# Performance work log

Measured on AMD Instinct MI355X. Metric: run time of the kernel, lower is better.

## Reference

```python
import jax, jax.numpy as jnp
import numpy as np

MI_N, DIS_N = 16384, 8192
EM = 128
E_MM, E_DD = MI_N * 32, DIS_N * 32


def _add_self_loops(edges, ew, n):
    loop = jnp.arange(n, dtype=edges.dtype)
    row = jnp.concatenate([edges[0], loop])
    col = jnp.concatenate([edges[1], loop])
    ew = jnp.concatenate([ew, jnp.ones((n,), ew.dtype)])
    return row, col, ew


def gcn_conv(x, edges, w, b, n, ew=None):
    # PyG GCNConv: symmetric gcn_norm with self-loops (fill 1.0), then
    # out[col] += norm * (x @ w)[row], plus bias.
    if ew is None:
        ew = jnp.ones((edges.shape[1],), x.dtype)
    row, col, ew = _add_self_loops(edges, ew, n)
    deg = jax.ops.segment_sum(ew, col, num_segments=n)
    dinv = jnp.where(deg > 0, jax.lax.rsqrt(deg), 0.0)
    norm = dinv[row] * ew * dinv[col]          # [E+n]
    h = x @ w                                   # [n, d]
    return jax.ops.segment_sum(h[row] * norm[:, None], col, num_segments=n) + b


def gat_conv(x, edges, w, a_src, a_dst, b, n):
    # PyG GATConv, heads=1: per-edge attention LeakyReLU(0.2) + softmax over
    # incoming edges of each target node (self-loops added).
    h = x @ w                                   # [n, d]
    row, col, _ = _add_self_loops(edges, jnp.ones((edges.shape[1],), x.dtype), n)
    e = jax.nn.leaky_relu((h @ a_src)[row] + (h @ a_dst)[col], negative_slope=0.2)
    m = jax.ops.segment_max(e, col, num_segments=n)
    ex = jnp.exp(e - m[col])
    s = jax.ops.segment_sum(ex, col, num_segments=n)
    alpha = ex / s[col]                         # [E+n]
    return jax.ops.segment_sum(h[row] * alpha[:, None], col, num_segments=n) + b


def setup_inputs() -> dict:
    key = jax.random.key(0)
    ks = jax.random.split(key, 24)
    sc = 1.0 / np.sqrt(EM)
    d = {
        'mm_x0': jax.random.normal(ks[0], (MI_N, EM), jnp.float32),
        'dd_x0': jax.random.normal(ks[1], (DIS_N, EM), jnp.float32),
        'w1_mm': jax.random.normal(ks[2], (EM, EM), jnp.float32) * sc,
        'b1_mm': jnp.zeros((EM,), jnp.float32),
        'w2_mm': jax.random.normal(ks[3], (EM, EM), jnp.float32) * sc,
        'b2_mm': jnp.zeros((EM,), jnp.float32),
        'w3_mm': jax.random.normal(ks[4], (EM, EM), jnp.float32) * sc,
        'asrc_mm': jax.random.normal(ks[5], (EM,), jnp.float32) * sc,
        'adst_mm': jax.random.normal(ks[6], (EM,), jnp.float32) * sc,
        'b3_mm': jnp.zeros((EM,), jnp.float32),
        'w1_dd': jax.random.normal(ks[7], (EM, EM), jnp.float32) * sc,
        'b1_dd': jnp.zeros((EM,), jnp.float32),
        'w2_dd': jax.random.normal(ks[8], (EM, EM), jnp.float32) * sc,
        'b2_dd': jnp.zeros((EM,), jnp.float32),
        'w3_dd': jax.random.normal(ks[9], (EM, EM), jnp.float32) * sc,
        'asrc_dd': jax.random.normal(ks[10], (EM,), jnp.float32) * sc,
        'adst_dd': jax.random.normal(ks[11], (EM,), jnp.float32) * sc,
        'b3_dd': jnp.zeros((EM,), jnp.float32),
        'mm_ew': jax.random.uniform(ks[12], (E_MM,), jnp.float32),
        'dd_ew': jax.random.uniform(ks[13], (E_DD,), jnp.float32),
        'mm_edges': jax.random.randint(ks[14], (2, E_MM), 0, MI_N, jnp.int32),
        'dd_edges': jax.random.randint(ks[15], (2, E_DD), 0, DIS_N, jnp.int32),
    }
    return d


def reference(mm_x0, dd_x0, w1_mm, b1_mm, w2_mm, b2_mm, w3_mm, asrc_mm, adst_mm,
              b3_mm, w1_dd, b1_dd, w2_dd, b2_dd, w3_dd, asrc_dd, adst_dd, b3_dd,
              mm_ew, dd_ew, mm_edges, dd_edges):
    elu = jax.nn.elu
    m1 = elu(gcn_conv(mm_x0, mm_edges, w1_mm, b1_mm, MI_N, mm_ew))
    m2 = elu(gcn_conv(m1, mm_edges, w2_mm, b2_mm, MI_N))
    m3 = elu(gat_conv(m2, mm_edges, w3_mm, asrc_mm, adst_mm, b3_mm, MI_N))
    d1 = elu(gcn_conv(dd_x0, dd_edges, w1_dd, b1_dd, DIS_N, dd_ew))
    d2 = elu(gcn_conv(d1, dd_edges, w2_dd, b2_dd, DIS_N))
    d3 = elu(gat_conv(d2, dd_edges, w3_dd, asrc_dd, adst_dd, b3_dd, DIS_N))
    mi_fea = (m1 + m2 + m3) / 3.0
    dis_fea = (d1 + d2 + d3) / 3.0
    score_raw = mi_fea @ dis_fea.T              # [MI_N, DIS_N]
    mn, mx = jnp.min(score_raw), jnp.max(score_raw)
    denom = jnp.where(mx > mn, mx - mn, jnp.asarray(1.0, score_raw.dtype))
    score_norm = jnp.where(mx > mn, (score_raw - mn) / denom,
                           jnp.zeros_like(score_raw))
    score_norm = jnp.clip(score_norm, 0.0, 1.0)
    return score_norm, mi_fea, dis_fea
```

## Files before the change

### kernel.cpp

```cpp
#include <hip/hip_runtime.h>
#include <cstdint>
#include <cstddef>

#define MI_NN 16384
#define DIS_NN 8192
#define EMB 128
#define EMM (MI_NN*32)
#define EDD (DIS_NN*32)

typedef __attribute__((ext_vector_type(8))) short short8;
typedef __attribute__((ext_vector_type(4))) float f32x4;

__device__ __forceinline__ float leakyr(float x){ return x > 0.f ? x : 0.2f*x; }
__device__ __forceinline__ float eluf(float x){ return x > 0.f ? x : expm1f(x); }

__device__ __forceinline__ unsigned bf16u(float x){
  unsigned u = __float_as_uint(x);
  return (u + 0x7FFFu + ((u >> 16) & 1u)) >> 16;
}
__device__ __forceinline__ float bfl(unsigned p){ return __uint_as_float(p << 16); }
__device__ __forceinline__ float bfh(unsigned p){ return __uint_as_float(p & 0xFFFF0000u); }

__global__ __launch_bounds__(256) void k_count2g(const int* __restrict__ c0, int* __restrict__ n0c,
                                                 int E0, int nb0,
                                                 const int* __restrict__ c1, int* __restrict__ n1c,
                                                 int E1){
  int b = blockIdx.x;
  const int* col; int* cnt; int E; int t;
  if (b < nb0){ col = c0; cnt = n0c; E = E0; t = b*256 + threadIdx.x; }
  else        { col = c1; cnt = n1c; E = E1; t = (b - nb0)*256 + threadIdx.x; }
  if (t < E) atomicAdd(&cnt[col[t]], 1);
}

__global__ __launch_bounds__(1024) void k_scan2g(const int* __restrict__ cnt0, int* __restrict__ rp0,
                                                 int n0, int E0,
                                                 const int* __restrict__ cnt1, int* __restrict__ rp1,
                                                 int n1, int E1){
  const int* cnt = blockIdx.x ? cnt1 : cnt0;
  int* rowptr    = blockIdx.x ? rp1  : rp0;
  int n          = blockIdx.x ? n1   : n0;
  int E          = blockIdx.x ? E1   : E0;
  __shared__ int lds[1024];
  int t = threadIdx.x;
  int chunk = n >> 10;
  int base = t*chunk;
  int s = 0;
  for (int i = 0; i < chunk; ++i) s += cnt[base+i];
  lds[t] = s; __syncthreads();
  for (int off = 1; off < 1024; off <<= 1){
    int v = (t >= off) ? lds[t-off] : 0;
    __syncthreads();
    lds[t] += v;
    __syncthreads();
  }
  int run = lds[t] - s;
  for (int i = 0; i < chunk; ++i){ rowptr[base+i] = run; run += cnt[base+i]; }
  if (t == 0) rowptr[n] = E;
}

__global__ __launch_bounds__(256) void k_fill2g(
    const int* __restrict__ r0a, const int* __restrict__ c0a, const float* __restrict__ w0a,
    const int* __restrict__ rp0, int* __restrict__ f0, int* __restrict__ s0, float* __restrict__ v0,
    int E0, int nb0,
    const int* __restrict__ r1a, const int* __restrict__ c1a, const float* __restrict__ w1a,
    const int* __restrict__ rp1, int* __restrict__ f1, int* __restrict__ s1, float* __restrict__ v1,
    int E1){
  int b = blockIdx.x;
  const int *row, *col; const float* ew; const int* rowptr;
  int *fill, *esrc; float* ewv; int E, t;
  if (b < nb0){ row=r0a; col=c0a; ew=w0a; rowptr=rp0; fill=f0; esrc=s0; ewv=v0; E=E0; t=b*256+threadIdx.x; }
  else        { row=r1a; col=c1a; ew=w1a; rowptr=rp1; fill=f1; esrc=s1; ewv=v1; E=E1; t=(b-nb0)*256+threadIdx.x; }
  if (t < E){
    int c = col[t];
    int p = rowptr[c] + atomicAdd(&fill[c], 1);
    esrc[p] = row[t];
    ewv[p] = ew[t];
  }
}

__global__ __launch_bounds__(256) void k_gemm2g(const float* __restrict__ X0, const float* __restrict__ W0,
                                                ushort* __restrict__ H0, int nb0,
                                                const float* __restrict__ X1, const float* __restrict__ W1,
                                                ushort* __restrict__ H1){
  int b = blockIdx.x;
  const float *X, *W; ushort* H; int rb;
  if (b < nb0){ X = X0; W = W0; H = H0; rb = b; }
  else        { X = X1; W = W1; H = H1; rb = b - nb0; }
  __shared__ float wl[EMB*EMB];
  int t = threadIdx.x;
  {
    const float4* W4 = (const float4*)W;
    float4* L4 = (float4*)wl;
    #pragma unroll
    for (int i = 0; i < 16; ++i) L4[t + 256*i] = W4[t + 256*i];
  }
  __syncthreads();
  int jg = t & 31;
  int rg = t >> 5;
  int r0 = rb*32 + rg*4;
  f32x4 acc0 = {0,0,0,0}, acc1 = {0,0,0,0}, acc2 = {0,0,0,0}, acc3 = {0,0,0,0};
  const float4* X4 = (const float4*)X;
  for (int k4 = 0; k4 < 32; ++k4){
    float4 x0 = X4[(size_t)(r0+0)*32 + k4];
    float4 x1 = X4[(size_t)(r0+1)*32 + k4];
    float4 x2 = X4[(size_t)(r0+2)*32 + k4];
    float4 x3 = X4[(size_t)(r0+3)*32 + k4];
#define GSTEP(c0,c1,c2,c3,kq) { f32x4 w4 = *(const f32x4*)&wl[(kq)*EMB + jg*4]; \
      acc0 += (c0)*w4; acc1 += (c1)*w4; acc2 += (c2)*w4; acc3 += (c3)*w4; }
    GSTEP(x0.x, x1.x, x2.x, x3.x, k4*4+0)
    GSTEP(x0.y, x1.y, x2.y, x3.y, k4*4+1)
    GSTEP(x0.z, x1.z, x2.z, x3.z, k4*4+2)
    GSTEP(x0.w, x1.w, x2.w, x3.w, k4*4+3)
#undef GSTEP
  }
#define PACK2(o, a) { o.x = bf16u(a[0]) | (bf16u(a[1])<<16); o.y = bf16u(a[2]) | (bf16u(a[3])<<16); }
  uint2 o0, o1, o2, o3;
  PACK2(o0, acc0) PACK2(o1, acc1) PACK2(o2, acc2) PACK2(o3, acc3)
#undef PACK2
  ushort* out = H + (size_t)r0*EMB + jg*4;
  *(uint2*)(out)         = o0;
  *(uint2*)(out + EMB)   = o1;
  *(uint2*)(out + 2*EMB) = o2;
  *(uint2*)(out + 3*EMB) = o3;
}

__global__ __launch_bounds__(256) void k_deg1_2g(const int* __restrict__ rp0, const float* __restrict__ ew0,
                                                 float* __restrict__ d0, int n0, int nb0,
                                                 const int* __restrict__ rp1, const float* __restrict__ ew1,
                                                 float* __restrict__ d1, int n1){
  int b = blockIdx.x;
  const int* rowptr; const float* ewv; float* dinv; int n, wid;
  int lane = threadIdx.x & 63;
  if (b < nb0){ rowptr=rp0; ewv=ew0; dinv=d0; n=n0; wid = (b*256 + threadIdx.x) >> 6; }
  else        { rowptr=rp1; ewv=ew1; dinv=d1; n=n1; wid = ((b-nb0)*256 + threadIdx.x) >> 6; }
  if (wid >= n) return;
  int beg = rowptr[wid], end = rowptr[wid+1];
  float s = 0.f;
  for (int i = beg + lane; i < end; i += 64) s += ewv[i];
  #pragma unroll
  for (int off = 32; off; off >>= 1) s += __shfl_xor(s, off);
  if (lane == 0) dinv[wid] = rsqrtf(1.0f + s);
}

__global__ __launch_bounds__(256) void k_deg2_2g(const int* __restrict__ rp0, float* __restrict__ d0,
                                                 int n0, int nb0,
                                                 const int* __restrict__ rp1, float* __restrict__ d1,
                                                 int n1){
  int b = blockIdx.x;
  const int* rowptr; float* dinv; int n, v;
  if (b < nb0){ rowptr=rp0; dinv=d0; n=n0; v = b*256 + threadIdx.x; }
  else        { rowptr=rp1; dinv=d1; n=n1; v = (b-nb0)*256 + threadIdx.x; }
  if (v < n) dinv[v] = rsqrtf(1.0f + (float)(rowptr[v+1] - rowptr[v]));
}

__global__ __launch_bounds__(256) void k_agg2g(
    const ushort* __restrict__ H0, const float* __restrict__ di0, const int* __restrict__ rp0,
    const int* __restrict__ sr0, const float* __restrict__ ew0, const float* __restrict__ bi0,
    float* __restrict__ xn0, float* __restrict__ fe0, int n0, int nb0,
    const ushort* __restrict__ H1, const float* __restrict__ di1, const int* __restrict__ rp1,
    const int* __restrict__ sr1, const float* __restrict__ ew1, const float* __restrict__ bi1,
    float* __restrict__ xn1, float* __restrict__ fe1, int n1,
    int femode){
  int b = blockIdx.x;
  const ushort* H; const float* dinv; const int* rowptr; const int* esrc;
  const float* ewv; const float* bias; float* xnext; float* fea; int n, wid;
  int lane = threadIdx.x & 63;
  if (b < nb0){ H=H0; dinv=di0; rowptr=rp0; esrc=sr0; ewv=ew0; bias=bi0; xnext=xn0; fea=fe0; n=n0;
                wid = (b*256 + threadIdx.x) >> 6; }
  else        { H=H1; dinv=di1; rowptr=rp1; esrc=sr1; ewv=ew1; bias=bi1; xnext=xn1; fea=fe1; n=n1;
                wid = ((b-nb0)*256 + threadIdx.x) >> 6; }
  if (wid >= n) return;
  int v = wid;
  float dv = dinv[v];
  unsigned hb = *(const unsigned*)(H + (size_t)v*EMB + lane*2);
  float ax = dv*bfl(hb), ay = dv*bfh(hb);
  int beg = rowptr[v], end = rowptr[v+1];
  int i = beg;
  int e4 = beg + ((end - beg) & ~3);
  for (; i < e4; i += 4){
    int r0 = esrc[i], r1 = esrc[i+1], r2 = esrc[i+2], r3 = esrc[i+3];
    float n0v = dinv[r0], n1v = dinv[r1], n2v = dinv[r2], n3v = dinv[r3];
    if (ewv){ n0v *= ewv[i]; n1v *= ewv[i+1]; n2v *= ewv[i+2]; n3v *= ewv[i+3]; }
    unsigned h0 = *(const unsigned*)(H + (size_t)r0*EMB + lane*2);
    unsigned h1 = *(const unsigned*)(H + (size_t)r1*EMB + lane*2);
    unsigned h2 = *(const unsigned*)(H + (size_t)r2*EMB + lane*2);
    unsigned h3 = *(const unsigned*)(H + (size_t)r3*EMB + lane*2);
    ax += n0v*bfl(h0) + n1v*bfl(h1) + n2v*bfl(h2) + n3v*bfl(h3);
    ay += n0v*bfh(h0) + n1v*bfh(h1) + n2v*bfh(h2) + n3v*bfh(h3);
  }
  for (; i < end; ++i){
    int r = esrc[i];
    float nm = dinv[r];
    if (ewv) nm *= ewv[i];
    unsigned hr = *(const unsigned*)(H + (size_t)r*EMB + lane*2);
    ax += nm*bfl(hr); ay += nm*bfh(hr);
  }
  float2 b2 = ((const float2*)bias)[lane];
  float ox = eluf(dv*ax + b2.x), oy = eluf(dv*ay + b2.y);
  ((float2*)xnext)[(size_t)v*64 + lane] = make_float2(ox, oy);
  float2* F2 = (float2*)fea;
  if (femode == 0){
    F2[(size_t)v*64 + lane] = make_float2(ox, oy);
  } else {
    float2 f = F2[(size_t)v*64 + lane];
    F2[(size_t)v*64 + lane] = make_float2(f.x + ox, f.y + oy);
  }
}

__global__ __launch_bounds__(256) void k_srcdst2g(
    const ushort* __restrict__ H0, const float* __restrict__ as0, const float* __restrict__ ad0,
    float* __restrict__ es0, float* __restrict__ ed0, int n0, int nb0,
    const ushort* __restrict__ H1, const float* __restrict__ as1, const float* __restrict__ ad1,
    float* __restrict__ es1, float* __restrict__ ed1, int n1){
  int b = blockIdx.x;
  const ushort* H; const float *asr, *ads; float *es, *ed; int n, wid;
  int lane = threadIdx.x & 63;
  if (b < nb0){ H=H0; asr=as0; ads=ad0; es=es0; ed=ed0; n=n0; wid = (b*256 + threadIdx.x) >> 6; }
  else        { H=H1; asr=as1; ads=ad1; es=es1; ed=ed1; n=n1; wid = ((b-nb0)*256 + threadIdx.x) >> 6; }
  if (wid >= n) return;
  unsigned hb = *(const unsigned*)(H + (size_t)wid*EMB + lane*2);
  float hx = bfl(hb), hy = bfh(hb);
  float2 s2 = ((const float2*)asr)[lane];
  float2 d2 = ((const float2*)ads)[lane];
  float ps = hx*s2.x + hy*s2.y;
  float pd = hx*d2.x + hy*d2.y;
  #pragma unroll
  for (int off = 32; off; off >>= 1){
    ps += __shfl_xor(ps, off);
    pd += __shfl_xor(pd, off);
  }
  if (lane == 0){ es[wid] = ps; ed[wid] = pd; }
}

__global__ __launch_bounds__(256) void k_gat2g(
    const ushort* __restrict__ H0, const float* __restrict__ es0, const float* __restrict__ ed0,
    const int* __restrict__ rp0, const int* __restrict__ sr0, const float* __restrict__ bi0,
    float* __restrict__ fe0, unsigned* __restrict__ sh0, int n0, int nb0,
    const ushort* __restrict__ H1, const float* __restrict__ es1, const float* __restrict__ ed1,
    const int* __restrict__ rp1, const int* __restrict__ sr1, const float* __restrict__ bi1,
    float* __restrict__ fe1, unsigned* __restrict__ sh1, int n1){
  int b = blockIdx.x;
  const ushort* H; const float *es, *ed; const int *rowptr, *esrc; const float* bias;
  float* fea; unsigned* shadow; int n, wid;
  int lane = threadIdx.x & 63;
  if (b < nb0){ H=H0; es=es0; ed=ed0; rowptr=rp0; esrc=sr0; bias=bi0; fea=fe0; shadow=sh0; n=n0;
                wid = (b*256 + threadIdx.x) >> 6; }
  else        { H=H1; es=es1; ed=ed1; rowptr=rp1; esrc=sr1; bias=bi1; fea=fe1; shadow=sh1; n=n1;
                wid = ((b-nb0)*256 + threadIdx.x) >> 6; }
  if (wid >= n) return;
  int v = wid;
  float edv = ed[v];
  float self_e = leakyr(es[v] + edv);
  int beg = rowptr[v], end = rowptr[v+1];
  float m = -3.4e38f, s = 0.f;
  for (int i = beg + lane; i < end; i += 64){
    float e = leakyr(es[esrc[i]] + edv);
    if (e > m){ s = s*expf(m - e) + 1.0f; m = e; }
    else s += expf(e - m);
  }
  #pragma unroll
  for (int off = 32; off; off >>= 1){
    float m2 = __shfl_xor(m, off), s2 = __shfl_xor(s, off);
    float mn_ = fmaxf(m, m2);
    s = s*expf(m - mn_) + s2*expf(m2 - mn_);
    m = mn_;
  }
  {
    float mn_ = fmaxf(m, self_e);
    s = s*expf(m - mn_) + expf(self_e - mn_);
    m = mn_;
  }
  float inv_s = 1.0f / s;
  unsigned hb = *(const unsigned*)(H + (size_t)v*EMB + lane*2);
  float a0 = expf(self_e - m)*inv_s;
  float ax = a0*bfl(hb), ay = a0*bfh(hb);
  int i = beg;
  int e4 = beg + ((end - beg) & ~3);
  for (; i < e4; i += 4){
    int r0 = esrc[i], r1 = esrc[i+1], r2 = esrc[i+2], r3 = esrc[i+3];
    float a_0 = expf(leakyr(es[r0] + edv) - m)*inv_s;
    float a_1 = expf(leakyr(es[r1] + edv) - m)*inv_s;
    float a_2 = expf(leakyr(es[r2] + edv) - m)*inv_s;
    float a_3 = expf(leakyr(es[r3] + edv) - m)*inv_s;
    unsigned h0 = *(const unsigned*)(H + (size_t)r0*EMB + lane*2);
    unsigned h1 = *(const unsigned*)(H + (size_t)r1*EMB + lane*2);
    unsigned h2 = *(const unsigned*)(H + (size_t)r2*EMB + lane*2);
    unsigned h3 = *(const unsigned*)(H + (size_t)r3*EMB + lane*2);
    ax += a_0*bfl(h0) + a_1*bfl(h1) + a_2*bfl(h2) + a_3*bfl(h3);
    ay += a_0*bfh(h0) + a_1*bfh(h1) + a_2*bfh(h2) + a_3*bfh(h3);
  }
  for (; i < end; ++i){
    int r = esrc[i];
    float a = expf(leakyr(es[r] + edv) - m)*inv_s;
    unsigned hr = *(const unsigned*)(H + (size_t)r*EMB + lane*2);
    ax += a*bfl(hr); ay += a*bfh(hr);
  }
  float2 b2 = ((const float2*)bias)[lane];
  float ox = eluf(ax + b2.x), oy = eluf(ay + b2.y);
  float2* F2 = (float2*)fea;
  float2 f = F2[(size_t)v*64 + lane];
  float fx = (f.x + ox)/3.0f, fy = (f.y + oy)/3.0f;
  F2[(size_t)v*64 + lane] = make_float2(fx, fy);
  shadow[(size_t)v*64 + lane] = bf16u(fx) | (bf16u(fy) << 16);
}

__device__ __forceinline__ void stage128(const uint8_t* G, uint8_t* L, int w, int lane){
  #pragma unroll
  for (int c = 0; c < 8; ++c){
    int linear = w*8192 + c*1024 + lane*16;
    int row = linear >> 8, col = linear & 255;
    const void* src = G + row*256 + (col ^ ((row & 7) << 4));
    __builtin_amdgcn_global_load_lds(
        (const __attribute__((address_space(1))) void*)src,
        (__attribute__((address_space(3))) void*)(L + w*8192 + c*1024),
        16, 0, 0);
  }
}

#define NT 16
template<int STORE>
__global__ __launch_bounds__(256) void k_score5(const ushort* __restrict__ Abf,
                                                const ushort* __restrict__ Bbf,
                                                float* __restrict__ S,
                                                float* __restrict__ mmpart){
  __shared__ __align__(16) uint8_t L0[32768];
  __shared__ __align__(16) uint8_t L1[32768];
  __shared__ float red[16];
  const int t = threadIdx.x;
  const int lane = t & 63;
  const int w = t >> 6;
  const int wr = w >> 1, wc = w & 1;
  const int lr = lane & 15, lk = lane >> 4;
  const int i0b = blockIdx.y * 128;
  const int jbase = blockIdx.x * NT;

  stage128((const uint8_t*)(Abf + (size_t)i0b*EMB), L0, w, lane);
  stage128((const uint8_t*)(Bbf + (size_t)jbase*128*EMB), L1, w, lane);
  __syncthreads();

  short8 af[4][4];
  #pragma unroll
  for (int at = 0; at < 4; ++at){
    int ra = wr*64 + at*16 + lr;
    #pragma unroll
    for (int k0 = 0; k0 < 4; ++k0){
      int kb = k0*64 + lk*16;
      af[at][k0] = *(const short8*)&L0[ra*256 + (kb ^ ((ra & 7) << 4))];
    }
  }
  __syncthreads();
  stage128((const uint8_t*)(Bbf + (size_t)(jbase+1)*128*EMB), L0, w, lane);

  float mn = 0.f, sc = 0.f;
  if (STORE){
    mn = mmpart[0];
    float mx = mmpart[1];
    sc = (mx > mn) ? 1.0f/(mx - mn) : 0.0f;
  }
  float lmin = 3.4e38f, lmax = -3.4e38f;

  for (int jt = 0; jt < NT; ++jt){
    uint8_t* curB = (jt & 1) ? L0 : L1;
    f32x4 acc[4][4];
    #pragma unroll
    for (int a = 0; a < 4; ++a)
      #pragma unroll
      for (int b = 0; b < 4; ++b) acc[a][b] = (f32x4){0.f,0.f,0.f,0.f};

    #pragma unroll
    for (int k0 = 0; k0 < 4; ++k0){
      int kb = k0*64 + lk*16;
      short8 bfr[4];
      #pragma unroll
      for (int ct = 0; ct < 4; ++ct){
        int rb = wc*64 + ct*16 + lr;
        bfr[ct] = *(const short8*)&curB[rb*256 + (kb ^ ((rb & 7) << 4))];
      }
      #pragma unroll
      for (int at = 0; at < 4; ++at)
        #pragma unroll
        for (int ct = 0; ct < 4; ++ct)
          acc[at][ct] = __builtin_amdgcn_mfma_f32_16x16x32_bf16(af[at][k0], bfr[ct], acc[at][ct], 0, 0, 0);
    }

    int j0 = (jbase + jt)*128;
    if (STORE){
      #pragma unroll
      for (int at = 0; at < 4; ++at){
        #pragma unroll
        for (int ct = 0; ct < 4; ++ct){
          int colj = j0 + wc*64 + ct*16 + lr;
          int row0 = i0b + wr*64 + at*16 + lk*4;
          #pragma unroll
          for (int q = 0; q < 4; ++q){
            float vv = fminf(fmaxf((acc[at][ct][q] - mn)*sc, 0.f), 1.f);
            S[(size_t)(row0+q)*DIS_NN + colj] = vv;
          }
        }
      }
    } else {
      #pragma unroll
      for (int at = 0; at < 4; ++at)
        #pragma unroll
        for (int ct = 0; ct < 4; ++ct)
          #pragma unroll
          for (int q = 0; q < 4; ++q){
            float vv = acc[at][ct][q];
            lmin = fminf(lmin, vv); lmax = fmaxf(lmax, vv);
          }
    }
    __syncthreads();
    if (jt + 2 < NT)
      stage128((const uint8_t*)(Bbf + (size_t)(jbase+jt+2)*128*EMB), curB, w, lane);
  }

  if (!STORE){
    #pragma unroll
    for (int off = 32; off; off >>= 1){
      lmin = fminf(lmin, __shfl_xor(lmin, off));
      lmax = fmaxf(lmax, __shfl_xor(lmax, off));
    }
    if (lane == 0){ red[w*2] = lmin; red[w*2+1] = lmax; }
    __syncthreads();
    if (t == 0){
      float a = fminf(fminf(red[0], red[2]), fminf(red[4], red[6]));
      float b = fmaxf(fmaxf(red[1], red[3]), fmaxf(red[5], red[7]));
      int bid = blockIdx.y * 4 + blockIdx.x;
      mmpart[2 + bid*2]     = a;
      mmpart[2 + bid*2 + 1] = b;
    }
  }
}

__global__ __launch_bounds__(512) void k_mmred(float* __restrict__ mm){
  __shared__ float2 red[8];
  int t = threadIdx.x;
  float mn = mm[2 + t*2];
  float mx = mm[2 + t*2 + 1];
  #pragma unroll
  for (int off = 32; off; off >>= 1){
    mn = fminf(mn, __shfl_xor(mn, off));
    mx = fmaxf(mx, __shfl_xor(mx, off));
  }
  if ((t & 63) == 0) red[t >> 6] = make_float2(mn, mx);
  __syncthreads();
  if (t == 0){
    float a = red[0].x, b = red[0].y;
    #pragma unroll
    for (int i = 1; i < 8; ++i){ a = fminf(a, red[i].x); b = fmaxf(b, red[i].y); }
    mm[0] = a; mm[1] = b;
  }
}

extern "C" void kernel_launch(void* const* d_in, const int* in_sizes, int n_in,
                              void* d_out, int out_size, void* d_ws, size_t ws_size,
                              hipStream_t stream){
  (void)in_sizes; (void)n_in; (void)out_size; (void)ws_size;
  const float* mm_x0  = (const float*)d_in[0];
  const float* dd_x0  = (const float*)d_in[1];
  const float* w1_mm  = (const float*)d_in[2];
  const float* b1_mm  = (const float*)d_in[3];
  const float* w2_mm  = (const float*)d_in[4];
  const float* b2_mm  = (const float*)d_in[5];
  const float* w3_mm  = (const float*)d_in[6];
  const float* asrc_mm= (const float*)d_in[7];
  const float* adst_mm= (const float*)d_in[8];
  const float* b3_mm  = (const float*)d_in[9];
  const float* w1_dd  = (const float*)d_in[10];
  const float* b1_dd  = (const float*)d_in[11];
  const float* w2_dd  = (const float*)d_in[12];
  const float* b2_dd  = (const float*)d_in[13];
  const float* w3_dd  = (const float*)d_in[14];
  const float* asrc_dd= (const float*)d_in[15];
  const float* adst_dd= (const float*)d_in[16];
  const float* b3_dd  = (const float*)d_in[17];
  const float* mm_ew  = (const float*)d_in[18];
  const float* dd_ew  = (const float*)d_in[19];
  const int* mm_edges = (const int*)d_in[20];
  const int* dd_edges = (const int*)d_in[21];

  float* S = (float*)d_out;
  float* p = S;
  float* A0m = p;  p += (size_t)MI_NN*EMB;
  float* A1m = p;  p += (size_t)MI_NN*EMB;
  float* A0d = p;  p += (size_t)DIS_NN*EMB;
  float* A1d = p;  p += (size_t)DIS_NN*EMB;
  ushort* Hbm = (ushort*)p; p += (size_t)MI_NN*EMB/2;
  ushort* Hbd = (ushort*)p; p += (size_t)DIS_NN*EMB/2;
  float* DEG1m = p; p += MI_NN;
  float* DEG2m = p; p += MI_NN;
  float* ESm   = p; p += MI_NN;
  float* EDm   = p; p += MI_NN;
  float* DEG1d = p; p += DIS_NN;
  float* DEG2d = p; p += DIS_NN;
  float* ESd   = p; p += DIS_NN;
  float* EDd   = p; p += DIS_NN;
  int* CNTm  = (int*)p; p += MI_NN;
  int* CNTd  = (int*)p; p += DIS_NN;
  int* FILLm = (int*)p; p += MI_NN;
  int* FILLd = (int*)p; p += DIS_NN;
  int* RPm   = (int*)p; p += MI_NN + 64;
  int* RPd   = (int*)p; p += DIS_NN + 64;
  int* ESRCm = (int*)p; p += EMM;
  int* ESRCd = (int*)p; p += EDD;
  float* EWVm = p; p += EMM;
  float* EWVd = p; p += EDD;
  float* FEA_MI  = S + (size_t)MI_NN * DIS_NN;
  float* FEA_DIS = FEA_MI + (size_t)MI_NN*EMB;

  float* MM = (float*)d_ws;
  ushort* Abf = (ushort*)((char*)d_ws + 16384);
  ushort* Bbf = Abf + (size_t)MI_NN * EMB;

  const int* erow_m = mm_edges;
  const int* ecol_m = mm_edges + EMM;
  const int* erow_d = dd_edges;
  const int* ecol_d = dd_edges + EDD;

  hipMemsetAsync(CNTm, 0, (size_t)(MI_NN + DIS_NN)*sizeof(int), stream);
  k_count2g<<<EMM/256 + EDD/256, 256, 0, stream>>>(ecol_m, CNTm, EMM, EMM/256,
                                                   ecol_d, CNTd, EDD);
  k_scan2g<<<2, 1024, 0, stream>>>(CNTm, RPm, MI_NN, EMM, CNTd, RPd, DIS_NN, EDD);
  hipMemsetAsync(FILLm, 0, (size_t)(MI_NN + DIS_NN)*sizeof(int), stream);
  k_fill2g<<<EMM/256 + EDD/256, 256, 0, stream>>>(erow_m, ecol_m, mm_ew, RPm, FILLm, ESRCm, EWVm,
                                                  EMM, EMM/256,
                                                  erow_d, ecol_d, dd_ew, RPd, FILLd, ESRCd, EWVd,
                                                  EDD);
  const int GB = MI_NN/32 + DIS_NN/32;
  const int AB = MI_NN/4 + DIS_NN/4;
  k_gemm2g<<<GB, 256, 0, stream>>>(mm_x0, w1_mm, Hbm, MI_NN/32, dd_x0, w1_dd, Hbd);
  k_deg1_2g<<<AB, 256, 0, stream>>>(RPm, EWVm, DEG1m, MI_NN, MI_NN/4, RPd, EWVd, DEG1d, DIS_NN);
  k_agg2g<<<AB, 256, 0, stream>>>(Hbm, DEG1m, RPm, ESRCm, EWVm, b1_mm, A0m, FEA_MI, MI_NN, MI_NN/4,
                                  Hbd, DEG1d, RPd, ESRCd, EWVd, b1_dd, A0d, FEA_DIS, DIS_NN, 0);
  k_gemm2g<<<GB, 256, 0, stream>>>(A0m, w2_mm, Hbm, MI_NN/32, A0d, w2_dd, Hbd);
  k_deg2_2g<<<MI_NN/256 + DIS_NN/256, 256, 0, stream>>>(RPm, DEG2m, MI_NN, MI_NN/256,
                                                        RPd, DEG2d, DIS_NN);
  k_agg2g<<<AB, 256, 0, stream>>>(Hbm, DEG2m, RPm, ESRCm, nullptr, b2_mm, A1m, FEA_MI, MI_NN, MI_NN/4,
                                  Hbd, DEG2d, RPd, ESRCd, nullptr, b2_dd, A1d, FEA_DIS, DIS_NN, 1);
  k_gemm2g<<<GB, 256, 0, stream>>>(A1m, w3_mm, Hbm, MI_NN/32, A1d, w3_dd, Hbd);
  k_srcdst2g<<<AB, 256, 0, stream>>>(Hbm, asrc_mm, adst_mm, ESm, EDm, MI_NN, MI_NN/4,
                                     Hbd, asrc_dd, adst_dd, ESd, EDd, DIS_NN);
  k_gat2g<<<AB, 256, 0, stream>>>(Hbm, ESm, EDm, RPm, ESRCm, b3_mm, FEA_MI, (unsigned*)Abf, MI_NN, MI_NN/4,
                                  Hbd, ESd, EDd, RPd, ESRCd, b3_dd, FEA_DIS, (unsigned*)Bbf, DIS_NN);
  k_score5<0><<<dim3(DIS_NN/(128*NT), MI_NN/128), 256, 0, stream>>>(Abf, Bbf, nullptr, MM);
  k_mmred<<<1, 512, 0, stream>>>(MM);
  k_score5<1><<<dim3(DIS_NN/(128*NT), MI_NN/128), 256, 0, stream>>>(Abf, Bbf, S, MM);
}
```

Before: 453.7 us.

## Pack CSR edges as int2, fuse GAT projections into GEMM, merge degree kernels

Edge source indices and weights are stored interleaved as int2 so each edge is fetched in a single load. The GAT src/dst attention projections are computed in the GEMM epilogue from fp32 accumulators, which removes a separate kernel. The two degree kernels are merged into one and the two memsets are combined. The large score output is written with nontemporal stores. Together these cut launches and memory traffic, but the projections now use unrounded fp32 values instead of bf16 H, which changes numerics slightly.

```diff
diff --git a/kernel.cpp b/kernel.cpp
--- a/kernel.cpp
+++ b/kernel.cpp
@@ -60,32 +60,34 @@
 
 __global__ __launch_bounds__(256) void k_fill2g(
     const int* __restrict__ r0a, const int* __restrict__ c0a, const float* __restrict__ w0a,
-    const int* __restrict__ rp0, int* __restrict__ f0, int* __restrict__ s0, float* __restrict__ v0,
+    const int* __restrict__ rp0, int* __restrict__ f0, int2* __restrict__ e0,
     int E0, int nb0,
     const int* __restrict__ r1a, const int* __restrict__ c1a, const float* __restrict__ w1a,
-    const int* __restrict__ rp1, int* __restrict__ f1, int* __restrict__ s1, float* __restrict__ v1,
+    const int* __restrict__ rp1, int* __restrict__ f1, int2* __restrict__ e1,
     int E1){
   int b = blockIdx.x;
   const int *row, *col; const float* ew; const int* rowptr;
-  int *fill, *esrc; float* ewv; int E, t;
-  if (b < nb0){ row=r0a; col=c0a; ew=w0a; rowptr=rp0; fill=f0; esrc=s0; ewv=v0; E=E0; t=b*256+threadIdx.x; }
-  else        { row=r1a; col=c1a; ew=w1a; rowptr=rp1; fill=f1; esrc=s1; ewv=v1; E=E1; t=(b-nb0)*256+threadIdx.x; }
+  int* fill; int2* epk; int E, t;
+  if (b < nb0){ row=r0a; col=c0a; ew=w0a; rowptr=rp0; fill=f0; epk=e0; E=E0; t=b*256+threadIdx.x; }
+  else        { row=r1a; col=c1a; ew=w1a; rowptr=rp1; fill=f1; epk=e1; E=E1; t=(b-nb0)*256+threadIdx.x; }
   if (t < E){
     int c = col[t];
     int p = rowptr[c] + atomicAdd(&fill[c], 1);
-    esrc[p] = row[t];
-    ewv[p] = ew[t];
-  }
-}
-
-__global__ __launch_bounds__(256) void k_gemm2g(const float* __restrict__ X0, const float* __restrict__ W0,
-                                                ushort* __restrict__ H0, int nb0,
-                                                const float* __restrict__ X1, const float* __restrict__ W1,
-                                                ushort* __restrict__ H1){
+    epk[p] = make_int2(row[t], __float_as_int(ew[t]));
+  }
+}
+
+__global__ __launch_bounds__(256) void k_gemm2g(
+    const float* __restrict__ X0, const float* __restrict__ W0, ushort* __restrict__ H0, int nb0,
+    const float* __restrict__ X1, const float* __restrict__ W1, ushort* __restrict__ H1,
+    const float* __restrict__ as0, const float* __restrict__ ad0,
+    float* __restrict__ es0, float* __restrict__ ed0,
+    const float* __restrict__ as1, const float* __restrict__ ad1,
+    float* __restrict__ es1, float* __restrict__ ed1){
   int b = blockIdx.x;
-  const float *X, *W; ushort* H; int rb;
-  if (b < nb0){ X = X0; W = W0; H = H0; rb = b; }
-  else        { X = X1; W = W1; H = H1; rb = b - nb0; }
+  const float *X, *W, *asr, *ads; ushort* H; float *es, *ed; int rb;
+  if (b < nb0){ X=X0; W=W0; H=H0; asr=as0; ads=ad0; es=es0; ed=ed0; rb = b; }
+  else        { X=X1; W=W1; H=H1; asr=as1; ads=ad1; es=es1; ed=ed1; rb = b - nb0; }
   __shared__ float wl[EMB*EMB];
   int t = threadIdx.x;
   {
@@ -122,52 +124,69 @@
   *(uint2*)(out + EMB)   = o1;
   *(uint2*)(out + 2*EMB) = o2;
   *(uint2*)(out + 3*EMB) = o3;
-}
-
-__global__ __launch_bounds__(256) void k_deg1_2g(const int* __restrict__ rp0, const float* __restrict__ ew0,
-                                                 float* __restrict__ d0, int n0, int nb0,
-                                                 const int* __restrict__ rp1, const float* __restrict__ ew1,
-                                                 float* __restrict__ d1, int n1){
+
+  if (asr){
+    f32x4 s4 = *(const f32x4*)&asr[jg*4];
+    f32x4 d4 = *(const f32x4*)&ads[jg*4];
+    float ps0 = acc0[0]*s4[0] + acc0[1]*s4[1] + acc0[2]*s4[2] + acc0[3]*s4[3];
+    float ps1 = acc1[0]*s4[0] + acc1[1]*s4[1] + acc1[2]*s4[2] + acc1[3]*s4[3];
+    float ps2 = acc2[0]*s4[0] + acc2[1]*s4[1] + acc2[2]*s4[2] + acc2[3]*s4[3];
+    float ps3 = acc3[0]*s4[0] + acc3[1]*s4[1] + acc3[2]*s4[2] + acc3[3]*s4[3];
+    float pd0 = acc0[0]*d4[0] + acc0[1]*d4[1] + acc0[2]*d4[2] + acc0[3]*d4[3];
+    float pd1 = acc1[0]*d4[0] + acc1[1]*d4[1] + acc1[2]*d4[2] + acc1[3]*d4[3];
+    float pd2 = acc2[0]*d4[0] + acc2[1]*d4[1] + acc2[2]*d4[2] + acc2[3]*d4[3];
+    float pd3 = acc3[0]*d4[0] + acc3[1]*d4[1] + acc3[2]*d4[2] + acc3[3]*d4[3];
+    #pragma unroll
+    for (int off = 16; off; off >>= 1){
+      ps0 += __shfl_xor(ps0, off); ps1 += __shfl_xor(ps1, off);
+      ps2 += __shfl_xor(ps2, off); ps3 += __shfl_xor(ps3, off);
+      pd0 += __shfl_xor(pd0, off); pd1 += __shfl_xor(pd1, off);
+      pd2 += __shfl_xor(pd2, off); pd3 += __shfl_xor(pd3, off);
+    }
+    if (jg == 0){
+      es[r0+0] = ps0; es[r0+1] = ps1; es[r0+2] = ps2; es[r0+3] = ps3;
+      ed[r0+0] = pd0; ed[r0+1] = pd1; ed[r0+2] = pd2; ed[r0+3] = pd3;
+    }
+  }
+}
+
+__global__ __launch_bounds__(256) void k_deg2g(
+    const int* __restrict__ rp0, const int2* __restrict__ ep0,
+    float* __restrict__ d10, float* __restrict__ d20, int n0, int nb0,
+    const int* __restrict__ rp1, const int2* __restrict__ ep1,
+    float* __restrict__ d11, float* __restrict__ d21, int n1){
   int b = blockIdx.x;
-  const int* rowptr; const float* ewv; float* dinv; int n, wid;
+  const int* rowptr; const int2* epk; float *d1, *d2; int n, wid;
   int lane = threadIdx.x & 63;
-  if (b < nb0){ rowptr=rp0; ewv=ew0; dinv=d0; n=n0; wid = (b*256 + threadIdx.x) >> 6; }
-  else        { rowptr=rp1; ewv=ew1; dinv=d1; n=n1; wid = ((b-nb0)*256 + threadIdx.x) >> 6; }
+  if (b < nb0){ rowptr=rp0; epk=ep0; d1=d10; d2=d20; n=n0; wid = (b*256 + threadIdx.x) >> 6; }
+  else        { rowptr=rp1; epk=ep1; d1=d11; d2=d21; n=n1; wid = ((b-nb0)*256 + threadIdx.x) >> 6; }
   if (wid >= n) return;
   int beg = rowptr[wid], end = rowptr[wid+1];
   float s = 0.f;
-  for (int i = beg + lane; i < end; i += 64) s += ewv[i];
+  for (int i = beg + lane; i < end; i += 64) s += __int_as_float(epk[i].y);
   #pragma unroll
   for (int off = 32; off; off >>= 1) s += __shfl_xor(s, off);
-  if (lane == 0) dinv[wid] = rsqrtf(1.0f + s);
-}
-
-__global__ __launch_bounds__(256) void k_deg2_2g(const int* __restrict__ rp0, float* __restrict__ d0,
-                                                 int n0, int nb0,
-                                                 const int* __restrict__ rp1, float* __restrict__ d1,
-                                                 int n1){
-  int b = blockIdx.x;
-  const int* rowptr; float* dinv; int n, v;
-  if (b < nb0){ rowptr=rp0; dinv=d0; n=n0; v = b*256 + threadIdx.x; }
-  else        { rowptr=rp1; dinv=d1; n=n1; v = (b-nb0)*256 + threadIdx.x; }
-  if (v < n) dinv[v] = rsqrtf(1.0f + (float)(rowptr[v+1] - rowptr[v]));
+  if (lane == 0){
+    d1[wid] = rsqrtf(1.0f + s);
+    d2[wid] = rsqrtf(1.0f + (float)(end - beg));
+  }
 }
 
 __global__ __launch_bounds__(256) void k_agg2g(
     const ushort* __restrict__ H0, const float* __restrict__ di0, const int* __restrict__ rp0,
-    const int* __restrict__ sr0, const float* __restrict__ ew0, const float* __restrict__ bi0,
+    const int2* __restrict__ ep0, const float* __restrict__ bi0,
     float* __restrict__ xn0, float* __restrict__ fe0, int n0, int nb0,
     const ushort* __restrict__ H1, const float* __restrict__ di1, const int* __restrict__ rp1,
-    const int* __restrict__ sr1, const float* __restrict__ ew1, const float* __restrict__ bi1,
+    const int2* __restrict__ ep1, const float* __restrict__ bi1,
     float* __restrict__ xn1, float* __restrict__ fe1, int n1,
-    int femode){
+    int useew, int femode){
   int b = blockIdx.x;
-  const ushort* H; const float* dinv; const int* rowptr; const int* esrc;
-  const float* ewv; const float* bias; float* xnext; float* fea; int n, wid;
+  const ushort* H; const float* dinv; const int* rowptr; const int2* epk;
+  const float* bias; float* xnext; float* fea; int n, wid;
   int lane = threadIdx.x & 63;
-  if (b < nb0){ H=H0; dinv=di0; rowptr=rp0; esrc=sr0; ewv=ew0; bias=bi0; xnext=xn0; fea=fe0; n=n0;
+  if (b < nb0){ H=H0; dinv=di0; rowptr=rp0; epk=ep0; bias=bi0; xnext=xn0; fea=fe0; n=n0;
                 wid = (b*256 + threadIdx.x) >> 6; }
-  else        { H=H1; dinv=di1; rowptr=rp1; esrc=sr1; ewv=ew1; bias=bi1; xnext=xn1; fea=fe1; n=n1;
+  else        { H=H1; dinv=di1; rowptr=rp1; epk=ep1; bias=bi1; xnext=xn1; fea=fe1; n=n1;
                 wid = ((b-nb0)*256 + threadIdx.x) >> 6; }
   if (wid >= n) return;
   int v = wid;
@@ -178,21 +197,22 @@
   int i = beg;
   int e4 = beg + ((end - beg) & ~3);
   for (; i < e4; i += 4){
-    int r0 = esrc[i], r1 = esrc[i+1], r2 = esrc[i+2], r3 = esrc[i+3];
-    float n0v = dinv[r0], n1v = dinv[r1], n2v = dinv[r2], n3v = dinv[r3];
-    if (ewv){ n0v *= ewv[i]; n1v *= ewv[i+1]; n2v *= ewv[i+2]; n3v *= ewv[i+3]; }
-    unsigned h0 = *(const unsigned*)(H + (size_t)r0*EMB + lane*2);
-    unsigned h1 = *(const unsigned*)(H + (size_t)r1*EMB + lane*2);
-    unsigned h2 = *(const unsigned*)(H + (size_t)r2*EMB + lane*2);
-    unsigned h3 = *(const unsigned*)(H + (size_t)r3*EMB + lane*2);
+    int2 e0 = epk[i], e1 = epk[i+1], e2 = epk[i+2], e3 = epk[i+3];
+    float n0v = dinv[e0.x], n1v = dinv[e1.x], n2v = dinv[e2.x], n3v = dinv[e3.x];
+    if (useew){ n0v *= __int_as_float(e0.y); n1v *= __int_as_float(e1.y);
+                n2v *= __int_as_float(e2.y); n3v *= __int_as_float(e3.y); }
+    unsigned h0 = *(const unsigned*)(H + (size_t)e0.x*EMB + lane*2);
+    unsigned h1 = *(const unsigned*)(H + (size_t)e1.x*EMB + lane*2);
+    unsigned h2 = *(const unsigned*)(H + (size_t)e2.x*EMB + lane*2);
+    unsigned h3 = *(const unsigned*)(H + (size_t)e3.x*EMB + lane*2);
     ax += n0v*bfl(h0) + n1v*bfl(h1) + n2v*bfl(h2) + n3v*bfl(h3);
     ay += n0v*bfh(h0) + n1v*bfh(h1) + n2v*bfh(h2) + n3v*bfh(h3);
   }
   for (; i < end; ++i){
-    int r = esrc[i];
-    float nm = dinv[r];
-    if (ewv) nm *= ewv[i];
-    unsigned hr = *(const unsigned*)(H + (size_t)r*EMB + lane*2);
+    int2 e = epk[i];
+    float nm = dinv[e.x];
+    if (useew) nm *= __int_as_float(e.y);
+    unsigned hr = *(const unsigned*)(H + (size_t)e.x*EMB + lane*2);
     ax += nm*bfl(hr); ay += nm*bfh(hr);
   }
   float2 b2 = ((const float2*)bias)[lane];
@@ -207,45 +227,20 @@
   }
 }
 
-__global__ __launch_bounds__(256) void k_srcdst2g(
-    const ushort* __restrict__ H0, const float* __restrict__ as0, const float* __restrict__ ad0,
-    float* __restrict__ es0, float* __restrict__ ed0, int n0, int nb0,
-    const ushort* __restrict__ H1, const float* __restrict__ as1, const float* __restrict__ ad1,
-    float* __restrict__ es1, float* __restrict__ ed1, int n1){
-  int b = blockIdx.x;
-  const ushort* H; const float *asr, *ads; float *es, *ed; int n, wid;
-  int lane = threadIdx.x & 63;
-  if (b < nb0){ H=H0; asr=as0; ads=ad0; es=es0; ed=ed0; n=n0; wid = (b*256 + threadIdx.x) >> 6; }
-  else        { H=H1; asr=as1; ads=ad1; es=es1; ed=ed1; n=n1; wid = ((b-nb0)*256 + threadIdx.x) >> 6; }
-  if (wid >= n) return;
-  unsigned hb = *(const unsigned*)(H + (size_t)wid*EMB + lane*2);
-  float hx = bfl(hb), hy = bfh(hb);
-  float2 s2 = ((const float2*)asr)[lane];
-  float2 d2 = ((const float2*)ads)[lane];
-  float ps = hx*s2.x + hy*s2.y;
-  float pd = hx*d2.x + hy*d2.y;
-  #pragma unroll
-  for (int off = 32; off; off >>= 1){
-    ps += __shfl_xor(ps, off);
-    pd += __shfl_xor(pd, off);
-  }
-  if (lane == 0){ es[wid] = ps; ed[wid] = pd; }
-}
-
 __global__ __launch_bounds__(256) void k_gat2g(
     const ushort* __restrict__ H0, const float* __restrict__ es0, const float* __restrict__ ed0,
-    const int* __restrict__ rp0, const int* __restrict__ sr0, const float* __restrict__ bi0,
+    const int* __restrict__ rp0, const int2* __restrict__ ep0, const float* __restrict__ bi0,
     float* __restrict__ fe0, unsigned* __restrict__ sh0, int n0, int nb0,
     const ushort* __restrict__ H1, const float* __restrict__ es1, const float* __restrict__ ed1,
-    const int* __restrict__ rp1, const int* __restrict__ sr1, const float* __restrict__ bi1,
+    const int* __restrict__ rp1, const int2* __restrict__ ep1, const float* __restrict__ bi1,
     float* __restrict__ fe1, unsigned* __restrict__ sh1, int n1){
   int b = blockIdx.x;
-  const ushort* H; const float *es, *ed; const int *rowptr, *esrc; const float* bias;
+  const ushort* H; const float *es, *ed; const int* rowptr; const int2* epk; const float* bias;
   float* fea; unsigned* shadow; int n, wid;
   int lane = threadIdx.x & 63;
-  if (b < nb0){ H=H0; es=es0; ed=ed0; rowptr=rp0; esrc=sr0; bias=bi0; fea=fe0; shadow=sh0; n=n0;
+  if (b < nb0){ H=H0; es=es0; ed=ed0; rowptr=rp0; epk=ep0; bias=bi0; fea=fe0; shadow=sh0; n=n0;
                 wid = (b*256 + threadIdx.x) >> 6; }
-  else        { H=H1; es=es1; ed=ed1; rowptr=rp1; esrc=sr1; bias=bi1; fea=fe1; shadow=sh1; n=n1;
+  else        { H=H1; es=es1; ed=ed1; rowptr=rp1; epk=ep1; bias=bi1; fea=fe1; shadow=sh1; n=n1;
                 wid = ((b-nb0)*256 + threadIdx.x) >> 6; }
   if (wid >= n) return;
   int v = wid;
@@ -254,7 +249,7 @@
   int beg = rowptr[v], end = rowptr[v+1];
   float m = -3.4e38f, s = 0.f;
   for (int i = beg + lane; i < end; i += 64){
-    float e = leakyr(es[esrc[i]] + edv);
+    float e = leakyr(es[epk[i].x] + edv);
     if (e > m){ s = s*expf(m - e) + 1.0f; m = e; }
     else s += expf(e - m);
   }
@@ -277,7 +272,7 @@
   int i = beg;
   int e4 = beg + ((end - beg) & ~3);
   for (; i < e4; i += 4){
-    int r0 = esrc[i], r1 = esrc[i+1], r2 = esrc[i+2], r3 = esrc[i+3];
+    int r0 = epk[i].x, r1 = epk[i+1].x, r2 = epk[i+2].x, r3 = epk[i+3].x;
     float a_0 = expf(leakyr(es[r0] + edv) - m)*inv_s;
     float a_1 = expf(leakyr(es[r1] + edv) - m)*inv_s;
     float a_2 = expf(leakyr(es[r2] + edv) - m)*inv_s;
@@ -290,7 +285,7 @@
     ay += a_0*bfh(h0) + a_1*bfh(h1) + a_2*bfh(h2) + a_3*bfh(h3);
   }
   for (; i < end; ++i){
-    int r = esrc[i];
+    int r = epk[i].x;
     float a = expf(leakyr(es[r] + edv) - m)*inv_s;
     unsigned hr = *(const unsigned*)(H + (size_t)r*EMB + lane*2);
     ax += a*bfl(hr); ay += a*bfh(hr);
@@ -394,7 +389,7 @@
           #pragma unroll
           for (int q = 0; q < 4; ++q){
             float vv = fminf(fmaxf((acc[at][ct][q] - mn)*sc, 0.f), 1.f);
-            S[(size_t)(row0+q)*DIS_NN + colj] = vv;
+            __builtin_nontemporal_store(vv, &S[(size_t)(row0+q)*DIS_NN + colj]);
           }
         }
       }
@@ -501,10 +496,8 @@
   int* FILLd = (int*)p; p += DIS_NN;
   int* RPm   = (int*)p; p += MI_NN + 64;
   int* RPd   = (int*)p; p += DIS_NN + 64;
-  int* ESRCm = (int*)p; p += EMM;
-  int* ESRCd = (int*)p; p += EDD;
-  float* EWVm = p; p += EMM;
-  float* EWVd = p; p += EDD;
+  int2* EPKm = (int2*)p; p += (size_t)EMM*2;
+  int2* EPKd = (int2*)p; p += (size_t)EDD*2;
   float* FEA_MI  = S + (size_t)MI_NN * DIS_NN;
   float* FEA_DIS = FEA_MI + (size_t)MI_NN*EMB;
 
@@ -517,31 +510,33 @@
   const int* erow_d = dd_edges;
   const int* ecol_d = dd_edges + EDD;
 
-  hipMemsetAsync(CNTm, 0, (size_t)(MI_NN + DIS_NN)*sizeof(int), stream);
+  hipMemsetAsync(CNTm, 0, (size_t)2*(MI_NN + DIS_NN)*sizeof(int), stream);
   k_count2g<<<EMM/256 + EDD/256, 256, 0, stream>>>(ecol_m, CNTm, EMM, EMM/256,
                                                    ecol_d, CNTd, EDD);
   k_scan2g<<<2, 1024, 0, stream>>>(CNTm, RPm, MI_NN, EMM, CNTd, RPd, DIS_NN, EDD);
-  hipMemsetAsync(FILLm, 0, (size_t)(MI_NN + DIS_NN)*sizeof(int), stream);
-  k_fill2g<<<EMM/256 + EDD/256, 256, 0, stream>>>(erow_m, ecol_m, mm_ew, RPm, FILLm, ESRCm, EWVm,
+  k_fill2g<<<EMM/256 + EDD/256, 256, 0, stream>>>(erow_m, ecol_m, mm_ew, RPm, FILLm, EPKm,
                                                   EMM, EMM/256,
-                                                  erow_d, ecol_d, dd_ew, RPd, FILLd, ESRCd, EWVd,
+                                                  erow_d, ecol_d, dd_ew, RPd, FILLd, EPKd,
                                                   EDD);
   const int GB = MI_NN/32 + DIS_NN/32;
   const int AB = MI_NN/4 + DIS_NN/4;
-  k_gemm2g<<<GB, 256, 0, stream>>>(mm_x0, w1_mm, Hbm, MI_NN/32, dd_x0, w1_dd, Hbd);
-  k_deg1_2g<<<AB, 256, 0, stream>>>(RPm, EWVm, DEG1m, MI_NN, MI_NN/4, RPd, EWVd, DEG1d, DIS_NN);
-  k_agg2g<<<AB, 256, 0, stream>>>(Hbm, DEG1m, RPm, ESRCm, EWVm, b1_mm, A0m, FEA_MI, MI_NN, MI_NN/4,
-                                  Hbd, DEG1d, RPd, ESRCd, EWVd, b1_dd, A0d, FEA_DIS, DIS_NN, 0);
-  k_gemm2g<<<GB, 256, 0, stream>>>(A0m, w2_mm, Hbm, MI_NN/32, A0d, w2_dd, Hbd);
-  k_deg2_2g<<<MI_NN/256 + DIS_NN/256, 256, 0, stream>>>(RPm, DEG2m, MI_NN, MI_NN/256,
-                                                        RPd, DEG2d, DIS_NN);
-  k_agg2g<<<AB, 256, 0, stream>>>(Hbm, DEG2m, RPm, ESRCm, nullptr, b2_mm, A1m, FEA_MI, MI_NN, MI_NN/4,
-                                  Hbd, DEG2d, RPd, ESRCd, nullptr, b2_dd, A1d, FEA_DIS, DIS_NN, 1);
-  k_gemm2g<<<GB, 256, 0, stream>>>(A1m, w3_mm, Hbm, MI_NN/32, A1d, w3_dd, Hbd);
-  k_srcdst2g<<<AB, 256, 0, stream>>>(Hbm, asrc_mm, adst_mm, ESm, EDm, MI_NN, MI_NN/4,
-                                     Hbd, asrc_dd, adst_dd, ESd, EDd, DIS_NN);
-  k_gat2g<<<AB, 256, 0, stream>>>(Hbm, ESm, EDm, RPm, ESRCm, b3_mm, FEA_MI, (unsigned*)Abf, MI_NN, MI_NN/4,
-                                  Hbd, ESd, EDd, RPd, ESRCd, b3_dd, FEA_DIS, (unsigned*)Bbf, DIS_NN);
+  k_gemm2g<<<GB, 256, 0, stream>>>(mm_x0, w1_mm, Hbm, MI_NN/32, dd_x0, w1_dd, Hbd,
+                                   nullptr, nullptr, nullptr, nullptr,
+                                   nullptr, nullptr, nullptr, nullptr);
+  k_deg2g<<<AB, 256, 0, stream>>>(RPm, EPKm, DEG1m, DEG2m, MI_NN, MI_NN/4,
+                                  RPd, EPKd, DEG1d, DEG2d, DIS_NN);
+  k_agg2g<<<AB, 256, 0, stream>>>(Hbm, DEG1m, RPm, EPKm, b1_mm, A0m, FEA_MI, MI_NN, MI_NN/4,
+                                  Hbd, DEG1d, RPd, EPKd, b1_dd, A0d, FEA_DIS, DIS_NN, 1, 0);
+  k_gemm2g<<<GB, 256, 0, stream>>>(A0m, w2_mm, Hbm, MI_NN/32, A0d, w2_dd, Hbd,
+                                   nullptr, nullptr, nullptr, nullptr,
+                                   nullptr, nullptr, nullptr, nullptr);
+  k_agg2g<<<AB, 256, 0, stream>>>(Hbm, DEG2m, RPm, EPKm, b2_mm, A1m, FEA_MI, MI_NN, MI_NN/4,
+                                  Hbd, DEG2d, RPd, EPKd, b2_dd, A1d, FEA_DIS, DIS_NN, 0, 1);
+  k_gemm2g<<<GB, 256, 0, stream>>>(A1m, w3_mm, Hbm, MI_NN/32, A1d, w3_dd, Hbd,
+                                   asrc_mm, adst_mm, ESm, EDm,
+                                   asrc_dd, adst_dd, ESd, EDd);
+  k_gat2g<<<AB, 256, 0, stream>>>(Hbm, ESm, EDm, RPm, EPKm, b3_mm, FEA_MI, (unsigned*)Abf, MI_NN, MI_NN/4,
+                                  Hbd, ESd, EDd, RPd, EPKd, b3_dd, FEA_DIS, (unsigned*)Bbf, DIS_NN);
   k_score5<0><<<dim3(DIS_NN/(128*NT), MI_NN/128), 256, 0, stream>>>(Abf, Bbf, nullptr, MM);
   k_mmred<<<1, 512, 0, stream>>>(MM);
   k_score5<1><<<dim3(DIS_NN/(128*NT), MI_NN/128), 256, 0, stream>>>(Abf, Bbf, S, MM);
```

Result: slower. 514.6 us (+13.4%).
